# Kernel tuning notes

Measured on AMD Instinct MI355X. Metric: run time of the kernel, lower is better.

## Reference

```python
import jax, jax.numpy as jnp
import numpy as np

BS, SEQ, DIM, NH = 2, 2048, 2048, 16
HD = DIM // NH  # 128


def setup_inputs() -> dict:
    key = jax.random.key(0)
    ks = jax.random.split(key, 6)
    x = jax.random.normal(ks[0], (BS, SEQ, DIM), dtype=jnp.float32)
    # rotary frequencies, theta=10000 as in LLaMA
    inv_freq = 1.0 / (10000.0 ** (jnp.arange(0, HD, 2, dtype=jnp.float32) / HD))  # [HD/2]
    t = jnp.arange(SEQ, dtype=jnp.float32)
    freqs = jnp.outer(t, inv_freq)  # [SEQ, HD/2]
    freqs_cos = jnp.cos(freqs)
    freqs_sin = jnp.sin(freqs)
    # additive causal mask [1,1,S,S]
    causal = jnp.tril(jnp.ones((SEQ, SEQ), dtype=bool))
    mask = jnp.where(causal, 0.0, -1e9).astype(jnp.float32)[None, None]
    scale = 0.02
    wq = jax.random.normal(ks[1], (DIM, DIM), dtype=jnp.float32) * scale
    wk = jax.random.normal(ks[2], (DIM, DIM), dtype=jnp.float32) * scale
    wv = jax.random.normal(ks[3], (DIM, DIM), dtype=jnp.float32) * scale
    wo = jax.random.normal(ks[4], (DIM, DIM), dtype=jnp.float32) * scale
    return {"x": x, "freqs_cos": freqs_cos, "freqs_sin": freqs_sin, "mask": mask,
            "wq": wq, "wk": wk, "wv": wv, "wo": wo}


def _apply_rope(t, cos, sin):
    # t: [b,s,h,hd]; cos/sin: [s,hd/2]
    tr = t.reshape(*t.shape[:-1], HD // 2, 2)
    tre, tim = tr[..., 0], tr[..., 1]
    c = cos[None, :, None, :]
    s = sin[None, :, None, :]
    out_re = tre * c - tim * s
    out_im = tre * s + tim * c
    return jnp.stack([out_re, out_im], axis=-1).reshape(t.shape)


def reference(x, freqs_cos, freqs_sin, mask, wq, wk, wv, wo):
    bs, seq, _ = x.shape
    q = (x @ wq).reshape(bs, seq, NH, HD)
    k = (x @ wk).reshape(bs, seq, NH, HD)
    v = (x @ wv).reshape(bs, seq, NH, HD)
    q = _apply_rope(q, freqs_cos, freqs_sin)
    k = _apply_rope(k, freqs_cos, freqs_sin)
    # [b,h,s,s]
    scores = jnp.einsum("bqhd,bkhd->bhqk", q, k) / np.sqrt(HD).astype(np.float32)
    scores = scores + mask
    probs = jax.nn.softmax(scores, axis=-1)
    out = jnp.einsum("bhqk,bkhd->bqhd", probs, v).reshape(bs, seq, DIM)
    return out @ wo
```

## Files before the change

### kernel.cpp

```cpp
#include <hip/hip_runtime.h>
#include <hip/hip_bf16.h>
#include <stdint.h>
#include <stddef.h>

#define SEQ 2048
#define DIM 2048
#define NH 16
#define HD 128
#define BSZ 2
#define MTOT (BSZ*SEQ)
#define KDIM 2048
#define NTL (KDIM/32)

typedef __bf16 bf16;
typedef __attribute__((ext_vector_type(4))) __bf16 bf16x4;
typedef __attribute__((ext_vector_type(8))) __bf16 bf16x8;
typedef __attribute__((ext_vector_type(4))) float f32x4;

#define MFMA16(a,b,c) __builtin_amdgcn_mfma_f32_16x16x32_bf16((a),(b),(c),0,0,0)

__device__ __forceinline__ void glds16(const void* g, void* l) {
  __builtin_amdgcn_global_load_lds((__attribute__((address_space(1))) void*)(g),
                                   (__attribute__((address_space(3))) void*)(l),
                                   16, 0, 0);
}

__device__ __forceinline__ f32x4 f4zero() { f32x4 v = {0.f, 0.f, 0.f, 0.f}; return v; }

__device__ __forceinline__ uint32_t bpack(float a, float b) {
  uint16_t au = __builtin_bit_cast(uint16_t, (bf16)a);
  uint16_t bu = __builtin_bit_cast(uint16_t, (bf16)b);
  return (uint32_t)au | ((uint32_t)bu << 16);
}

__global__ void cast_x_bf16(const float* __restrict__ in, bf16* __restrict__ out) {
  size_t i = (size_t)blockIdx.x * blockDim.x + threadIdx.x;
  float4 v = ((const float4*)in)[i];
  bf16x4 ov;
  ov.x = (bf16)v.x; ov.y = (bf16)v.y; ov.z = (bf16)v.z; ov.w = (bf16)v.w;
  ((bf16x4*)out)[i] = ov;
}

__global__ void transpose_w(const float* __restrict__ W, bf16* __restrict__ WT) {
  __shared__ float tile[64][65];
  const int bk = blockIdx.x, bn = blockIdx.y;
  const int tid = threadIdx.x;
  const int tc = tid & 15, tr = tid >> 4;
#pragma unroll
  for (int p = 0; p < 4; ++p) {
    int k = tr + p * 16;
    float4 v = *(const float4*)(W + (size_t)(bk * 64 + k) * DIM + bn * 64 + tc * 4);
    tile[k][tc * 4 + 0] = v.x;
    tile[k][tc * 4 + 1] = v.y;
    tile[k][tc * 4 + 2] = v.z;
    tile[k][tc * 4 + 3] = v.w;
  }
  __syncthreads();
#pragma unroll
  for (int p = 0; p < 4; ++p) {
    int n = tr + p * 16;
    bf16x4 ov;
    ov.x = (bf16)tile[tc * 4 + 0][n];
    ov.y = (bf16)tile[tc * 4 + 1][n];
    ov.z = (bf16)tile[tc * 4 + 2][n];
    ov.w = (bf16)tile[tc * 4 + 3][n];
    *(bf16x4*)(WT + (size_t)(bn * 64 + n) * DIM + bk * 64 + tc * 4) = ov;
  }
}

template<int MODE>
__global__ __launch_bounds__(512, 2)
void gemm9(const bf16* __restrict__ A, const bf16* __restrict__ BT,
           float* __restrict__ out0,
           bf16* __restrict__ qb, bf16* __restrict__ kbuf, bf16* __restrict__ vT,
           const float* __restrict__ cosT, const float* __restrict__ sinT)
{
  extern __shared__ uint8_t smem[];
  const int tid = threadIdx.x;
  const int lane = tid & 63, w = tid >> 6;
  const int l15 = lane & 15, h4 = lane >> 4;
  const int wr = w & 3, wc = w >> 2;

  const int f = blockIdx.x;
  const int cpx = gridDim.x >> 3;
  const int swz = (f & 7) * cpx + (f >> 3);
  const int bm = swz & 15;
  const int bn = swz >> 4;

  const size_t strideB = (size_t)KDIM * 2;
  const uint8_t* Ab = (const uint8_t*)A + (size_t)(bm * 256) * strideB;
  const uint8_t* Bb = (const uint8_t*)BT + (size_t)(bn * 128) * strideB;

  const int r0 = tid >> 2;
  const int g0 = tid & 3;

  auto stage = [&](int t) {
    uint8_t* slot = smem + (t & 3) * 24576;
    const int k0 = t * 64;
    int row = r0;
    glds16(Ab + (size_t)row * strideB + k0 + ((g0 ^ ((row >> 1) & 3)) << 4),
           slot + tid * 16);
    row = 128 + r0;
    glds16(Ab + (size_t)row * strideB + k0 + ((g0 ^ ((row >> 1) & 3)) << 4),
           slot + 8192 + tid * 16);
    row = r0;
    glds16(Bb + (size_t)row * strideB + k0 + ((g0 ^ ((row >> 1) & 3)) << 4),
           slot + 16384 + tid * 16);
  };

  f32x4 acc[4][4];
#pragma unroll
  for (int m = 0; m < 4; ++m)
#pragma unroll
    for (int n = 0; n < 4; ++n) acc[m][n] = f4zero();

  stage(0); stage(1); stage(2);
  asm volatile("s_waitcnt vmcnt(6)" ::: "memory");
  __builtin_amdgcn_s_barrier();
  asm volatile("" ::: "memory");

#pragma unroll 1
  for (int p = 0; p < NTL; ++p) {
    const uint8_t* sa = smem + (p & 3) * 24576;
    const uint8_t* sb = sa + 16384;
    bf16x8 aF[4], bF[4];
#pragma unroll
    for (int mf = 0; mf < 4; ++mf) {
      int row = wr * 64 + mf * 16 + l15;
      aF[mf] = *(const bf16x8*)(sa + row * 64 + ((h4 ^ ((row >> 1) & 3)) << 4));
    }
#pragma unroll
    for (int nf = 0; nf < 4; ++nf) {
      int row = wc * 64 + nf * 16 + l15;
      bF[nf] = *(const bf16x8*)(sb + row * 64 + ((h4 ^ ((row >> 1) & 3)) << 4));
    }
    if (p + 3 < NTL) stage(p + 3);

    asm volatile("" ::: "memory");
    __builtin_amdgcn_s_barrier();
    asm volatile("" ::: "memory");

    __builtin_amdgcn_s_setprio(1);
#pragma unroll
    for (int mf = 0; mf < 4; ++mf)
#pragma unroll
      for (int nf = 0; nf < 4; ++nf)
        acc[mf][nf] = MFMA16(aF[mf], bF[nf], acc[mf][nf]);
    __builtin_amdgcn_s_setprio(0);

    if (p < NTL - 3)       { asm volatile("s_waitcnt vmcnt(6)" ::: "memory"); }
    else if (p == NTL - 3) { asm volatile("s_waitcnt vmcnt(3)" ::: "memory"); }
    else if (p == NTL - 2) { asm volatile("s_waitcnt vmcnt(0)" ::: "memory"); }
    asm volatile("" ::: "memory");
    __builtin_amdgcn_s_barrier();
    asm volatile("" ::: "memory");
  }

  const int row0 = bm * 256 + wr * 64;
  const int col0 = bn * 128 + wc * 64;
#pragma unroll
  for (int mf = 0; mf < 4; ++mf) {
#pragma unroll
    for (int nf = 0; nf < 4; ++nf) {
#pragma unroll
      for (int r = 0; r < 4; ++r) {
        int row = row0 + mf * 16 + h4 * 4 + r;
        int col = col0 + nf * 16 + l15;
        float v = acc[mf][nf][r];
        if constexpr (MODE == 0) {
          out0[(size_t)row * DIM + col] = v;
        } else {
          int seg = col >> 11;
          int ccol = col & (DIM - 1);
          if (seg < 2) {
            float v2 = __shfl_xor(v, 1);
            int s = row & (SEQ - 1);
            int jidx = (ccol & (HD - 1)) >> 1;
            float c = cosT[s * (HD / 2) + jidx];
            float sn = sinT[s * (HD / 2) + jidx];
            float o = (col & 1) ? fmaf(v2, sn, v * c) : fmaf(v, c, -(v2 * sn));
            bf16* dst = (seg == 0) ? qb : kbuf;
            dst[(size_t)row * DIM + ccol] = (bf16)o;
          } else {
            int hh = ccol >> 7, d = ccol & (HD - 1);
            int bb = row >> 11, s = row & (SEQ - 1);
            vT[((size_t)(bb * NH + hh) * HD + d) * SEQ + s] = (bf16)v;
          }
        }
      }
    }
  }
}

__global__ __launch_bounds__(256, 2)
void flash_attn(const bf16* __restrict__ Q, const bf16* __restrict__ Kg,
                const bf16* __restrict__ VT, bf16* __restrict__ O)
{
  __shared__ __align__(16) bf16 Ks[2][64 * 128];
  __shared__ __align__(16) bf16 Vs[2][128 * 64];

  const int fidx = blockIdx.x;
  const int xr = fidx & 7, inner = fidx >> 3;
  const int pr = inner & 15;
  const int g = xr + 8 * (inner >> 4);
  const int h = g & 15, b = g >> 4;

  const int tid = threadIdx.x, lane = tid & 63, w = tid >> 6;
  const int l15 = lane & 15, h4 = lane >> 4;
  const bool hhalf = ((h4 >> 1) & 1) != 0;

  const float scale = 0.08838834764831845f;
  const uint8_t* kgb = (const uint8_t*)Kg + ((size_t)(b * SEQ) * DIM + h * HD) * 2;
  const uint8_t* vgb = (const uint8_t*)VT + ((size_t)(b * NH + h) * HD * SEQ) * 2;

  auto stageKV = [&](int buf, int t) {
    const uint8_t* ksrc = kgb + (size_t)t * 64 * (DIM * 2);
    const uint8_t* vsrc = vgb + (size_t)t * 64 * 2;
#pragma unroll
    for (int j = 0; j < 4; ++j) {
      int chunk = w * 256 + j * 64 + lane;
      int key = chunk >> 4, ck = chunk & 15;
      int jk = (ck * 16) ^ ((key & 7) << 4);
      glds16(ksrc + (size_t)key * (DIM * 2) + jk,
             (uint8_t*)&Ks[buf][0] + (w * 256 + j * 64) * 16);
      int d = chunk >> 3, cv = chunk & 7;
      int jv = (cv * 16) ^ ((d & 7) << 4);
      glds16(vsrc + (size_t)d * (SEQ * 2) + jv,
             (uint8_t*)&Vs[buf][0] + (w * 256 + j * 64) * 16);
    }
  };

#pragma unroll 1
  for (int qsel = 0; qsel < 2; ++qsel) {
    const int qt = qsel ? (SEQ / 64 - 1 - pr) : pr;
    const int q0 = qt * 64;
    const int qrow = q0 + w * 16 + l15;

    const bf16* qbase = Q + ((size_t)(b * SEQ + qrow)) * DIM + h * HD;
    bf16x8 aQ[4];
#pragma unroll
    for (int kk = 0; kk < 4; ++kk)
      aQ[kk] = *(const bf16x8*)(qbase + kk * 32 + h4 * 8);

    f32x4 o[8];
#pragma unroll
    for (int i = 0; i < 8; ++i) o[i] = f4zero();
    float mrun = -1e30f, lrun = 0.0f;

    stageKV(0, 0);
    __syncthreads();

#pragma unroll 1
    for (int t = 0; t <= qt; ++t) {
      const int cur = t & 1;
      if (t < qt) stageKV(cur ^ 1, t + 1);

      f32x4 S[4];
      __builtin_amdgcn_s_setprio(1);
#pragma unroll
      for (int kb = 0; kb < 4; ++kb) {
        f32x4 a = f4zero();
        int key = kb * 16 + l15;
        int swzk = (key & 7) << 4;
#pragma unroll
        for (int kk = 0; kk < 4; ++kk) {
          bf16x8 aK = *(const bf16x8*)((const uint8_t*)&Ks[cur][0] + key * 256 +
                                       (((kk * 32 + h4 * 8) * 2) ^ swzk));
          a = MFMA16(aK, aQ[kk], a);
        }
        S[kb] = a;
      }
      __builtin_amdgcn_s_setprio(0);

      if (t == qt) {
#pragma unroll
        for (int kb = 0; kb < 4; ++kb)
#pragma unroll
          for (int r = 0; r < 4; ++r) {
            int key = q0 + kb * 16 + h4 * 4 + r;
            float sv = S[kb][r] * scale;
            S[kb][r] = (key > qrow) ? -1e9f : sv;
          }
      } else {
#pragma unroll
        for (int kb = 0; kb < 4; ++kb)
#pragma unroll
          for (int r = 0; r < 4; ++r) S[kb][r] *= scale;
      }

      float pmax = S[0][0];
#pragma unroll
      for (int kb = 0; kb < 4; ++kb)
#pragma unroll
        for (int r = 0; r < 4; ++r) pmax = fmaxf(pmax, S[kb][r]);
      pmax = fmaxf(pmax, __shfl_xor(pmax, 16));
      pmax = fmaxf(pmax, __shfl_xor(pmax, 32));
      float mnew = fmaxf(mrun, pmax);
      float corr = __expf(mrun - mnew);
      float p[4][4];
      float psum = 0.f;
#pragma unroll
      for (int kb = 0; kb < 4; ++kb)
#pragma unroll
        for (int r = 0; r < 4; ++r) {
          float pv = __expf(S[kb][r] - mnew);
          p[kb][r] = pv;
          psum += pv;
        }
      psum += __shfl_xor(psum, 16);
      psum += __shfl_xor(psum, 32);
      lrun = lrun * corr + psum;
      mrun = mnew;
#pragma unroll
      for (int i = 0; i < 8; ++i) o[i] *= corr;

      uint32_t pk[4][2];
#pragma unroll
      for (int kb = 0; kb < 4; ++kb) {
        pk[kb][0] = bpack(p[kb][0], p[kb][1]);
        pk[kb][1] = bpack(p[kb][2], p[kb][3]);
      }

      bf16x8 pB[2];
#pragma unroll
      for (int kb2 = 0; kb2 < 2; ++kb2) {
        uint32_t s0a = hhalf ? pk[kb2 * 2 + 1][0] : pk[kb2 * 2][0];
        uint32_t s0b = hhalf ? pk[kb2 * 2 + 1][1] : pk[kb2 * 2][1];
        uint32_t s1a = hhalf ? pk[kb2 * 2][0] : pk[kb2 * 2 + 1][0];
        uint32_t s1b = hhalf ? pk[kb2 * 2][1] : pk[kb2 * 2 + 1][1];
        uint32_t e16a = __shfl_xor(s0a, 16), e16b = __shfl_xor(s0b, 16);
        uint32_t e32a = __shfl_xor(s1a, 32), e32b = __shfl_xor(s1b, 32);
        uint32_t e48a = __shfl_xor(s1a, 48), e48b = __shfl_xor(s1b, 48);
        uint32_t lo0 = (h4 == 0) ? s0a : (h4 == 1) ? e48a : (h4 == 2) ? e32a : e16a;
        uint32_t lo1 = (h4 == 0) ? s0b : (h4 == 1) ? e48b : (h4 == 2) ? e32b : e16b;
        uint32_t hi0 = (h4 == 0) ? e16a : (h4 == 1) ? e32a : (h4 == 2) ? e48a : s0a;
        uint32_t hi1 = (h4 == 0) ? e16b : (h4 == 1) ? e32b : (h4 == 2) ? e48b : s0b;
        uint4 u = make_uint4(lo0, lo1, hi0, hi1);
        pB[kb2] = __builtin_bit_cast(bf16x8, u);
      }

      __builtin_amdgcn_s_setprio(1);
#pragma unroll
      for (int db = 0; db < 8; ++db) {
        int drow = db * 16 + l15;
        int swzv = (drow & 7) << 4;
#pragma unroll
        for (int kb2 = 0; kb2 < 2; ++kb2) {
          bf16x8 aV = *(const bf16x8*)((const uint8_t*)&Vs[cur][0] + drow * 128 +
                                       (((kb2 * 32 + h4 * 8) * 2) ^ swzv));
          o[db] = MFMA16(aV, pB[kb2], o[db]);
        }
      }
      __builtin_amdgcn_s_setprio(0);

      __syncthreads();
    }

    float inv = 1.0f / lrun;
    bf16* obase = O + ((size_t)(b * SEQ + qrow)) * DIM + h * HD;
#pragma unroll
    for (int db = 0; db < 8; ++db) {
      uint32_t w0 = bpack(o[db][0] * inv, o[db][1] * inv);
      uint32_t w1 = bpack(o[db][2] * inv, o[db][3] * inv);
      uint2 st = make_uint2(w0, w1);
      *(uint2*)(obase + db * 16 + h4 * 4) = st;
    }
  }
}

extern "C" void kernel_launch(void* const* d_in, const int* in_sizes, int n_in,
                              void* d_out, int out_size, void* d_ws, size_t ws_size,
                              hipStream_t stream)
{
  const float* x    = (const float*)d_in[0];
  const float* fcos = (const float*)d_in[1];
  const float* fsin = (const float*)d_in[2];
  const float* wq   = (const float*)d_in[4];
  const float* wk   = (const float*)d_in[5];
  const float* wv   = (const float*)d_in[6];
  const float* wo   = (const float*)d_in[7];

  uint8_t* ws = (uint8_t*)d_ws;
  const size_t SZ_XB = (size_t)MTOT * DIM * 2;
  const size_t SZ_WT = (size_t)DIM * DIM * 2;

  bf16* xb    = (bf16*)(ws);
  bf16* wqT   = (bf16*)(ws + SZ_XB);
  bf16* wkT   = (bf16*)(ws + SZ_XB + 1 * SZ_WT);
  bf16* wvT   = (bf16*)(ws + SZ_XB + 2 * SZ_WT);
  bf16* woT   = (bf16*)(ws + SZ_XB + 3 * SZ_WT);
  bf16* qb    = (bf16*)(ws + SZ_XB + 4 * SZ_WT);
  bf16* kb    = (bf16*)(ws + 2 * SZ_XB + 4 * SZ_WT);
  bf16* vT    = (bf16*)(ws + 3 * SZ_XB + 4 * SZ_WT);
  bf16* attnb = xb;

  hipFuncSetAttribute((const void*)gemm9<1>,
                      hipFuncAttributeMaxDynamicSharedMemorySize, 98304);
  hipFuncSetAttribute((const void*)gemm9<0>,
                      hipFuncAttributeMaxDynamicSharedMemorySize, 98304);

  cast_x_bf16<<<(MTOT * DIM) / (256 * 4), 256, 0, stream>>>(x, xb);
  dim3 tg(DIM / 64, DIM / 64);
  transpose_w<<<tg, 256, 0, stream>>>(wq, wqT);
  transpose_w<<<tg, 256, 0, stream>>>(wk, wkT);
  transpose_w<<<tg, 256, 0, stream>>>(wv, wvT);
  transpose_w<<<tg, 256, 0, stream>>>(wo, woT);

  gemm9<1><<<768, 512, 98304, stream>>>(xb, wqT, nullptr, qb, kb, vT, fcos, fsin);

  flash_attn<<<512, 256, 0, stream>>>(qb, kb, vT, attnb);

  gemm9<0><<<256, 512, 98304, stream>>>(attnb, woT, (float*)d_out,
                                        nullptr, nullptr, nullptr, nullptr, nullptr);
}
```

Measured before the change: 427.9 us.

## Use 4-wave GEMM blocks with 128x64 per-wave tiles and 3-stage pipeline

Shrinks the GEMM workgroup from 8 to 4 waves, keeping the 256x128 block tile. Each wave now computes a 128x64 sub-tile with 8x4 MFMA fragments, which cuts LDS fragment reads per MFMA and raises per-wave arithmetic intensity. The LDS ring drops from 4 to 3 stages, each thread issues 6 async loads per stage, and the barrier that sat before the MFMA block is removed so only one barrier remains per k-step. The costs are many more accumulator registers per wave, a shallower prefetch depth and fewer waves available to hide memory latency.

```diff
diff --git a/kernel.cpp b/kernel.cpp
--- a/kernel.cpp
+++ b/kernel.cpp
@@ -69,17 +69,18 @@
 }
 
 template<int MODE>
-__global__ __launch_bounds__(512, 2)
-void gemm9(const bf16* __restrict__ A, const bf16* __restrict__ BT,
-           float* __restrict__ out0,
-           bf16* __restrict__ qb, bf16* __restrict__ kbuf, bf16* __restrict__ vT,
-           const float* __restrict__ cosT, const float* __restrict__ sinT)
+__global__ __launch_bounds__(256, 2)
+void gemm10(const bf16* __restrict__ A, const bf16* __restrict__ BT,
+            float* __restrict__ out0,
+            bf16* __restrict__ qb, bf16* __restrict__ kbuf, bf16* __restrict__ vT,
+            const float* __restrict__ cosT, const float* __restrict__ sinT)
 {
   extern __shared__ uint8_t smem[];
   const int tid = threadIdx.x;
-  const int lane = tid & 63, w = tid >> 6;
+  const int lane = tid & 63;
+  const int w = tid >> 6;
   const int l15 = lane & 15, h4 = lane >> 4;
-  const int wr = w & 3, wc = w >> 2;
+  const int wm = w & 1, wn = w >> 1;
 
   const int f = blockIdx.x;
   const int cpx = gridDim.x >> 3;
@@ -91,75 +92,74 @@
   const uint8_t* Ab = (const uint8_t*)A + (size_t)(bm * 256) * strideB;
   const uint8_t* Bb = (const uint8_t*)BT + (size_t)(bn * 128) * strideB;
 
-  const int r0 = tid >> 2;
-  const int g0 = tid & 3;
-
   auto stage = [&](int t) {
-    uint8_t* slot = smem + (t & 3) * 24576;
+    uint8_t* slot = smem + (t % 3) * 24576;
     const int k0 = t * 64;
-    int row = r0;
-    glds16(Ab + (size_t)row * strideB + k0 + ((g0 ^ ((row >> 1) & 3)) << 4),
-           slot + tid * 16);
-    row = 128 + r0;
-    glds16(Ab + (size_t)row * strideB + k0 + ((g0 ^ ((row >> 1) & 3)) << 4),
-           slot + 8192 + tid * 16);
-    row = r0;
-    glds16(Bb + (size_t)row * strideB + k0 + ((g0 ^ ((row >> 1) & 3)) << 4),
-           slot + 16384 + tid * 16);
+#pragma unroll
+    for (int i = 0; i < 4; ++i) {
+      int chunk = i * 256 + tid;
+      int row = chunk >> 2, c = chunk & 3;
+      int cs = c ^ ((row >> 1) & 3);
+      glds16(Ab + (size_t)row * strideB + k0 + (cs << 4), slot + chunk * 16);
+    }
+#pragma unroll
+    for (int i = 0; i < 2; ++i) {
+      int chunk = i * 256 + tid;
+      int row = chunk >> 2, c = chunk & 3;
+      int cs = c ^ ((row >> 1) & 3);
+      glds16(Bb + (size_t)row * strideB + k0 + (cs << 4),
+             slot + 16384 + chunk * 16);
+    }
   };
 
-  f32x4 acc[4][4];
-#pragma unroll
-  for (int m = 0; m < 4; ++m)
+  f32x4 acc[8][4];
+#pragma unroll
+  for (int m = 0; m < 8; ++m)
 #pragma unroll
     for (int n = 0; n < 4; ++n) acc[m][n] = f4zero();
 
-  stage(0); stage(1); stage(2);
+  stage(0); stage(1);
   asm volatile("s_waitcnt vmcnt(6)" ::: "memory");
   __builtin_amdgcn_s_barrier();
   asm volatile("" ::: "memory");
 
 #pragma unroll 1
   for (int p = 0; p < NTL; ++p) {
-    const uint8_t* sa = smem + (p & 3) * 24576;
+    const uint8_t* sa = smem + (p % 3) * 24576;
     const uint8_t* sb = sa + 16384;
-    bf16x8 aF[4], bF[4];
-#pragma unroll
-    for (int mf = 0; mf < 4; ++mf) {
-      int row = wr * 64 + mf * 16 + l15;
+    bf16x8 aF[8], bF[4];
+#pragma unroll
+    for (int mf = 0; mf < 8; ++mf) {
+      int row = wm * 128 + mf * 16 + l15;
       aF[mf] = *(const bf16x8*)(sa + row * 64 + ((h4 ^ ((row >> 1) & 3)) << 4));
     }
 #pragma unroll
     for (int nf = 0; nf < 4; ++nf) {
-      int row = wc * 64 + nf * 16 + l15;
+      int row = wn * 64 + nf * 16 + l15;
       bF[nf] = *(const bf16x8*)(sb + row * 64 + ((h4 ^ ((row >> 1) & 3)) << 4));
     }
-    if (p + 3 < NTL) stage(p + 3);
-
-    asm volatile("" ::: "memory");
-    __builtin_amdgcn_s_barrier();
-    asm volatile("" ::: "memory");
+    if (p + 2 < NTL) stage(p + 2);
 
     __builtin_amdgcn_s_setprio(1);
 #pragma unroll
-    for (int mf = 0; mf < 4; ++mf)
+    for (int mf = 0; mf < 8; ++mf)
 #pragma unroll
       for (int nf = 0; nf < 4; ++nf)
         acc[mf][nf] = MFMA16(aF[mf], bF[nf], acc[mf][nf]);
     __builtin_amdgcn_s_setprio(0);
 
-    if (p < NTL - 3)       { asm volatile("s_waitcnt vmcnt(6)" ::: "memory"); }
-    else if (p == NTL - 3) { asm volatile("s_waitcnt vmcnt(3)" ::: "memory"); }
+    if (p < NTL - 2)       { asm volatile("s_waitcnt vmcnt(6)" ::: "memory"); }
     else if (p == NTL - 2) { asm volatile("s_waitcnt vmcnt(0)" ::: "memory"); }
-    asm volatile("" ::: "memory");
-    __builtin_amdgcn_s_barrier();
-    asm volatile("" ::: "memory");
+    if (p < NTL - 1) {
+      __builtin_amdgcn_s_barrier();
+      asm volatile("" ::: "memory");
+    }
   }
 
-  const int row0 = bm * 256 + wr * 64;
-  const int col0 = bn * 128 + wc * 64;
-#pragma unroll
-  for (int mf = 0; mf < 4; ++mf) {
+  const int row0 = bm * 256 + wm * 128;
+  const int col0 = bn * 128 + wn * 64;
+#pragma unroll
+  for (int mf = 0; mf < 8; ++mf) {
 #pragma unroll
     for (int nf = 0; nf < 4; ++nf) {
 #pragma unroll
@@ -394,10 +394,10 @@
   bf16* vT    = (bf16*)(ws + 3 * SZ_XB + 4 * SZ_WT);
   bf16* attnb = xb;
 
-  hipFuncSetAttribute((const void*)gemm9<1>,
-                      hipFuncAttributeMaxDynamicSharedMemorySize, 98304);
-  hipFuncSetAttribute((const void*)gemm9<0>,
-                      hipFuncAttributeMaxDynamicSharedMemorySize, 98304);
+  hipFuncSetAttribute((const void*)gemm10<1>,
+                      hipFuncAttributeMaxDynamicSharedMemorySize, 73728);
+  hipFuncSetAttribute((const void*)gemm10<0>,
+                      hipFuncAttributeMaxDynamicSharedMemorySize, 73728);
 
   cast_x_bf16<<<(MTOT * DIM) / (256 * 4), 256, 0, stream>>>(x, xb);
   dim3 tg(DIM / 64, DIM / 64);
@@ -406,10 +406,10 @@
   transpose_w<<<tg, 256, 0, stream>>>(wv, wvT);
   transpose_w<<<tg, 256, 0, stream>>>(wo, woT);
 
-  gemm9<1><<<768, 512, 98304, stream>>>(xb, wqT, nullptr, qb, kb, vT, fcos, fsin);
+  gemm10<1><<<768, 256, 73728, stream>>>(xb, wqT, nullptr, qb, kb, vT, fcos, fsin);
 
   flash_attn<<<512, 256, 0, stream>>>(qb, kb, vT, attnb);
 
-  gemm9<0><<<256, 512, 98304, stream>>>(attnb, woT, (float*)d_out,
-                                        nullptr, nullptr, nullptr, nullptr, nullptr);
-}
+  gemm10<0><<<256, 256, 73728, stream>>>(attnb, woT, (float*)d_out,
+                                         nullptr, nullptr, nullptr, nullptr, nullptr);
+}
```

Result: slower. 436.8 us (+2.1%).
